# Kernel optimization log

Measured on AMD Instinct MI355X. Metric: run time of the kernel, lower is better.

Reference implementation:

```python
import jax, jax.numpy as jnp
import numpy as np

DIM = 1024
MLP_DIM = 4096
EPS = 1e-5


def layer_norm(x, gamma, beta):
    mean = jnp.mean(x, axis=-1, keepdims=True)
    var = jnp.mean(jnp.square(x - mean), axis=-1, keepdims=True)  # unbiased=False
    return gamma * (x - mean) / jnp.sqrt(var + EPS) + beta


def setup_inputs() -> dict:
    key = jax.random.key(0)
    ks = jax.random.split(key, 12)
    s = 0.02
    return {
        "x": jax.random.normal(ks[0], (4, 2048, DIM), dtype=jnp.float32),
        "gamma1": jnp.ones((DIM,), jnp.float32),
        "beta1": jnp.zeros((DIM,), jnp.float32),
        "gamma2": jnp.ones((DIM,), jnp.float32),
        "beta2": jnp.zeros((DIM,), jnp.float32),
        "Wq": jax.random.normal(ks[1], (DIM, DIM), jnp.float32) * s,
        "bq": jnp.zeros((DIM,), jnp.float32),
        "Wk": jax.random.normal(ks[2], (DIM, DIM), jnp.float32) * s,
        "bk": jnp.zeros((DIM,), jnp.float32),
        "Wv": jax.random.normal(ks[3], (DIM, DIM), jnp.float32) * s,
        "bv": jnp.zeros((DIM,), jnp.float32),
        "W1": jax.random.normal(ks[4], (DIM, MLP_DIM), jnp.float32) * s,
        "b1": jnp.zeros((MLP_DIM,), jnp.float32),
        "W2": jax.random.normal(ks[5], (MLP_DIM, DIM), jnp.float32) * s,
        "b2": jnp.zeros((DIM,), jnp.float32),
    }


def reference(x, gamma1, beta1, gamma2, beta2, Wq, bq, Wk, bk, Wv, bv, W1, b1, W2, b2):
    # Pre-LN attention sub-block (single-head manual attention over full dim)
    residual = x
    h = layer_norm(x, gamma1, beta1)
    q = h @ Wq + bq  # [B,S,D]
    k = h @ Wk + bk
    v = h @ Wv + bv
    scale = 1.0 / jnp.sqrt(jnp.asarray(q.shape[-1], q.dtype))
    scores = jnp.einsum("bsd,btd->bst", q, k) * scale  # [B,S,S]
    attn = jax.nn.softmax(scores, axis=-1)
    x = jnp.einsum("bst,btd->bsd", attn, v) + residual
    # Pre-LN MLP sub-block
    residual = x
    h = layer_norm(x, gamma2, beta2)
    h = jax.nn.gelu(h @ W1 + b1, approximate=False)  # torch F.gelu exact
    x = h @ W2 + b2 + residual
    return x
```

## Files before the change

### kernel.cpp

```cpp
#include <hip/hip_runtime.h>
#include <hip/hip_bf16.h>
#include <math.h>

typedef __bf16 bf16x8 __attribute__((ext_vector_type(8)));
typedef float  f32x4  __attribute__((ext_vector_type(4)));
typedef __hip_bfloat16 bf16;

#define DIM  1024
#define MLPD 4096
#define NB   4
#define SEQ  2048
#define ROWS (NB * SEQ)

__device__ __forceinline__ void gload_lds16(const void* g, void* l) {
  __builtin_amdgcn_global_load_lds(
      (__attribute__((address_space(1))) void*)(g),
      (__attribute__((address_space(3))) void*)(l), 16, 0, 0);
}

__device__ __forceinline__ void bar() {
  asm volatile("" ::: "memory");
  __builtin_amdgcn_s_barrier();
  asm volatile("" ::: "memory");
}

__device__ __forceinline__ void vm0() {
  asm volatile("s_waitcnt vmcnt(0)" ::: "memory");
}

__device__ __forceinline__ bf16 to_bf16(float v) { return __float2bfloat16(v); }
__device__ __forceinline__ bf16 to_bf16(bf16 v)  { return v; }

template <int EPI>
__global__ __launch_bounds__(256, 4) void gemm128(
    const bf16* __restrict__ A,  long aBatch, int lda,
    const bf16* __restrict__ Bt, long bBatch, int ldb,
    void* __restrict__ Cout,     long cBatch, int ldc,
    const float* __restrict__ bias,
    const float* __restrict__ resid, long rBatch, int ldr,
    int K, float scale)
{
  __shared__ char smem[2][16384];

  const int gx = gridDim.x, gy = gridDim.y;
  const int n = gx * gy * gridDim.z;
  const int f = blockIdx.x + gx * (blockIdx.y + gy * blockIdx.z);
  const int o = (f & 7) * (n >> 3) + (f >> 3);
  const int sx = gx >> 3;
  int st = o >> 6;
  const int w = o & 63;
  const int spz = sx * (gy >> 3);
  const int bz = st / spz; st -= bz * spz;
  const int sty = st / sx, stx = st - sty * sx;
  const int by = sty * 8 + (w >> 3), bx = stx * 8 + (w & 7);

  const long rowBase = (long)by * 128;
  const long colBase = (long)bx * 128;
  const long ldaB = (long)lda * 2, ldbB = (long)ldb * 2;
  const char* Ag = (const char*)(A + bz * aBatch + rowBase * lda);
  const char* Bg = (const char*)(Bt + bz * bBatch + colBase * ldb);

  const int tid  = threadIdx.x;
  const int lane = tid & 63;
  const int wave = tid >> 6;
  const int wm = wave >> 1, wn = wave & 1;
  const int fr = lane & 15, fq = lane >> 4;

  const int sslot = (fq ^ (fr & 3)) << 4;
  const int abase = ((wm * 64 + fr) << 6) + sslot;
  const int bbase = ((wn * 64 + fr) << 6) + sslot + 8192;

  const int c0   = wave * 2;
  const int swz  = ((lane & 3) ^ ((lane >> 2) & 3)) << 4;
  const int srow = lane >> 2;
  const char* aSrc0 = Ag + (long)(c0 * 16 + srow) * ldaB + swz;
  const char* aSrc1 = aSrc0 + 16 * ldaB;
  const char* bSrc0 = Bg + (long)(c0 * 16 + srow) * ldbB + swz;
  const char* bSrc1 = bSrc0 + 16 * ldbB;
  const int doff = c0 * 1024 + lane * 16;

  const int NT = K >> 5;
  f32x4 acc[4][4] = {};

#define STAGE(WB)                                                              \
  do {                                                                         \
    gload_lds16(aSrc0, &smem[WB][doff]);                                       \
    gload_lds16(aSrc1, &smem[WB][doff + 1024]);                                \
    gload_lds16(bSrc0, &smem[WB][8192 + doff]);                                \
    gload_lds16(bSrc1, &smem[WB][8192 + doff + 1024]);                         \
    aSrc0 += 64; aSrc1 += 64; bSrc0 += 64; bSrc1 += 64;                        \
  } while (0)

#define TILE(T, RB, WB)                                                        \
  do {                                                                         \
    if ((T) + 1 < NT) STAGE(WB);                                               \
    bf16x8 av[4], bv[4];                                                       \
    _Pragma("unroll") for (int m = 0; m < 4; ++m)                              \
      av[m] = *(const bf16x8*)(&smem[RB][0] + abase + m * 1024);               \
    _Pragma("unroll") for (int nn = 0; nn < 4; ++nn)                           \
      bv[nn] = *(const bf16x8*)(&smem[RB][0] + bbase + nn * 1024);             \
    __builtin_amdgcn_s_setprio(1);                                             \
    _Pragma("unroll") for (int m = 0; m < 4; ++m)                              \
      _Pragma("unroll") for (int nn = 0; nn < 4; ++nn)                         \
        acc[m][nn] = __builtin_amdgcn_mfma_f32_16x16x32_bf16(                  \
            av[m], bv[nn], acc[m][nn], 0, 0, 0);                               \
    __builtin_amdgcn_s_setprio(0);                                             \
    vm0(); bar();                                                              \
  } while (0)

  STAGE(0);
  vm0(); bar();

  for (int t = 0; t < NT; t += 2) {
    TILE(t, 0, 1);
    TILE(t + 1, 1, 0);
  }

#undef STAGE
#undef TILE

#pragma unroll
  for (int m = 0; m < 4; ++m) {
#pragma unroll
    for (int nn = 0; nn < 4; ++nn) {
      const long col = colBase + wn * 64 + nn * 16 + fr;
#pragma unroll
      for (int e = 0; e < 4; ++e) {
        const long r = rowBase + wm * 64 + m * 16 + fq * 4 + e;
        float v = acc[m][nn][e];
        if constexpr (EPI == 0) {
          v += bias[col];
          ((bf16*)Cout)[bz * cBatch + r * ldc + col] = __float2bfloat16(v);
        } else if constexpr (EPI == 1) {
          ((float*)Cout)[bz * cBatch + r * ldc + col] = v * scale;
        } else if constexpr (EPI == 2) {
          v += resid[bz * rBatch + r * ldr + col];
          ((float*)Cout)[bz * cBatch + r * ldc + col] = v;
        } else if constexpr (EPI == 3) {
          v += bias[col];
          const float gl = 0.5f * v * (1.0f + erff(v * 0.70710678118654752f));
          ((bf16*)Cout)[bz * cBatch + r * ldc + col] = __float2bfloat16(gl);
        } else {
          v += bias[col] + resid[r * (long)ldr + col];
          ((float*)Cout)[bz * cBatch + r * ldc + col] = v;
        }
      }
    }
  }
}

__global__ __launch_bounds__(256) void ln_kernel(
    const float* __restrict__ x, const float* __restrict__ gamma,
    const float* __restrict__ beta, bf16* __restrict__ out)
{
  const long row = blockIdx.x;
  const float4 v = ((const float4*)(x + row * DIM))[threadIdx.x];
  float s  = v.x + v.y + v.z + v.w;
  float ss = v.x * v.x + v.y * v.y + v.z * v.z + v.w * v.w;
  const int lane = threadIdx.x & 63, wave = threadIdx.x >> 6;
#pragma unroll
  for (int o = 32; o; o >>= 1) { s += __shfl_xor(s, o); ss += __shfl_xor(ss, o); }
  __shared__ float rs[4], rss[4];
  if (lane == 0) { rs[wave] = s; rss[wave] = ss; }
  __syncthreads();
  s  = rs[0] + rs[1] + rs[2] + rs[3];
  ss = rss[0] + rss[1] + rss[2] + rss[3];
  const float mean = s * (1.0f / DIM);
  const float var  = ss * (1.0f / DIM) - mean * mean;
  const float rstd = rsqrtf(var + 1e-5f);
  const float4 g = ((const float4*)gamma)[threadIdx.x];
  const float4 b = ((const float4*)beta)[threadIdx.x];
  union { bf16 h[4]; uint2 u; } pk;
  pk.h[0] = __float2bfloat16(g.x * (v.x - mean) * rstd + b.x);
  pk.h[1] = __float2bfloat16(g.y * (v.y - mean) * rstd + b.y);
  pk.h[2] = __float2bfloat16(g.z * (v.z - mean) * rstd + b.z);
  pk.h[3] = __float2bfloat16(g.w * (v.w - mean) * rstd + b.w);
  ((uint2*)(out + row * DIM))[threadIdx.x] = pk.u;
}

__global__ __launch_bounds__(256) void softmax_kernel(float* __restrict__ scores)
{
  const long row = blockIdx.x;
  float* rp = scores + row * (long)SEQ;
  const float4 v0 = ((const float4*)rp)[threadIdx.x * 2];
  const float4 v1 = ((const float4*)rp)[threadIdx.x * 2 + 1];
  float f[8] = {v0.x, v0.y, v0.z, v0.w, v1.x, v1.y, v1.z, v1.w};
  const int lane = threadIdx.x & 63, wave = threadIdx.x >> 6;
  float mx = f[0];
#pragma unroll
  for (int j = 1; j < 8; ++j) mx = fmaxf(mx, f[j]);
#pragma unroll
  for (int o = 32; o; o >>= 1) mx = fmaxf(mx, __shfl_xor(mx, o));
  __shared__ float rm[4], rsum[4];
  if (lane == 0) rm[wave] = mx;
  __syncthreads();
  mx = fmaxf(fmaxf(rm[0], rm[1]), fmaxf(rm[2], rm[3]));
  float sum = 0.0f;
#pragma unroll
  for (int j = 0; j < 8; ++j) { f[j] = expf(f[j] - mx); sum += f[j]; }
#pragma unroll
  for (int o = 32; o; o >>= 1) sum += __shfl_xor(sum, o);
  if (lane == 0) rsum[wave] = sum;
  __syncthreads();
  sum = rsum[0] + rsum[1] + rsum[2] + rsum[3];
  const float inv = 1.0f / sum;
  union { bf16 h[8]; uint4 u; } pk;
#pragma unroll
  for (int j = 0; j < 8; ++j) pk.h[j] = __float2bfloat16(f[j] * inv);
  bf16* prow = (bf16*)scores + row * (long)(2 * SEQ);
  ((uint4*)prow)[threadIdx.x] = pk.u;
}

template <typename TI>
__global__ __launch_bounds__(256) void transpose_bf16_kernel(
    const TI* __restrict__ in, bf16* __restrict__ out,
    int ldIn, int ldOut, long inBatch, long outBatch)
{
  __shared__ bf16 tile[32][33];
  const long zin  = (long)blockIdx.z * inBatch;
  const long zout = (long)blockIdx.z * outBatch;
  const int c0 = blockIdx.x * 32, r0 = blockIdx.y * 32;
  const int tx = threadIdx.x & 31, ty = threadIdx.x >> 5;
#pragma unroll
  for (int i = 0; i < 32; i += 8)
    tile[ty + i][tx] = to_bf16(in[zin + (long)(r0 + ty + i) * ldIn + c0 + tx]);
  __syncthreads();
#pragma unroll
  for (int i = 0; i < 32; i += 8)
    out[zout + (long)(c0 + ty + i) * ldOut + r0 + tx] = tile[tx][ty + i];
}

__global__ __launch_bounds__(256) void concat3_kernel(
    const float* __restrict__ a, const float* __restrict__ b,
    const float* __restrict__ c, float* __restrict__ o)
{
  const int i = blockIdx.x * 256 + threadIdx.x;
  if (i < DIM) { o[i] = a[i]; o[DIM + i] = b[i]; o[2 * DIM + i] = c[i]; }
}

extern "C" void kernel_launch(void* const* d_in, const int* in_sizes, int n_in,
                              void* d_out, int out_size, void* d_ws, size_t ws_size,
                              hipStream_t stream) {
  const float* x   = (const float*)d_in[0];
  const float* g1  = (const float*)d_in[1];
  const float* be1 = (const float*)d_in[2];
  const float* g2  = (const float*)d_in[3];
  const float* be2 = (const float*)d_in[4];
  const float* Wq  = (const float*)d_in[5];
  const float* bq  = (const float*)d_in[6];
  const float* Wk  = (const float*)d_in[7];
  const float* bk  = (const float*)d_in[8];
  const float* Wv  = (const float*)d_in[9];
  const float* bv  = (const float*)d_in[10];
  const float* W1  = (const float*)d_in[11];
  const float* b1  = (const float*)d_in[12];
  const float* W2  = (const float*)d_in[13];
  const float* b2  = (const float*)d_in[14];
  float* out = (float*)d_out;

  char* ws = (char*)d_ws;
  bf16* WqkvT = (bf16*)(ws + 0);
  bf16* W1T   = (bf16*)(ws + (6l << 20));
  bf16* W2T   = (bf16*)(ws + (14l << 20));
  float* bqkv = (float*)(ws + (22l << 20));
  bf16* h     = (bf16*)(ws + (23l << 20));
  bf16* qkv   = (bf16*)(ws + (39l << 20));
  bf16* vT    = (bf16*)(ws + (87l << 20));
  float* sc   = (float*)(ws + (103l << 20));
  bf16* P     = (bf16*)sc;
  bf16* g_act = (bf16*)sc;

  const dim3 blk(256);

  concat3_kernel<<<4, blk, 0, stream>>>(bq, bk, bv, bqkv);
  transpose_bf16_kernel<float><<<dim3(32, 32, 1), blk, 0, stream>>>(
      Wq, WqkvT, DIM, DIM, 0, 0);
  transpose_bf16_kernel<float><<<dim3(32, 32, 1), blk, 0, stream>>>(
      Wk, WqkvT + (long)DIM * DIM, DIM, DIM, 0, 0);
  transpose_bf16_kernel<float><<<dim3(32, 32, 1), blk, 0, stream>>>(
      Wv, WqkvT + 2l * DIM * DIM, DIM, DIM, 0, 0);
  transpose_bf16_kernel<float><<<dim3(128, 32, 1), blk, 0, stream>>>(
      W1, W1T, MLPD, DIM, 0, 0);
  transpose_bf16_kernel<float><<<dim3(32, 128, 1), blk, 0, stream>>>(
      W2, W2T, DIM, MLPD, 0, 0);

  ln_kernel<<<ROWS, blk, 0, stream>>>(x, g1, be1, h);

  gemm128<0><<<dim3(24, 64, 1), blk, 0, stream>>>(
      h, 0, DIM, WqkvT, 0, DIM, qkv, 0, 3 * DIM,
      bqkv, nullptr, 0, 0, DIM, 1.0f);

  transpose_bf16_kernel<bf16><<<dim3(32, 64, NB), blk, 0, stream>>>(
      qkv + 2 * DIM, vT, 3 * DIM, SEQ, (long)SEQ * 3 * DIM, (long)DIM * SEQ);

  gemm128<1><<<dim3(16, 16, NB), blk, 0, stream>>>(
      qkv, (long)SEQ * 3 * DIM, 3 * DIM, qkv + DIM, (long)SEQ * 3 * DIM, 3 * DIM,
      sc, (long)SEQ * SEQ, SEQ, nullptr, nullptr, 0, 0, DIM, 0.03125f);

  softmax_kernel<<<ROWS, blk, 0, stream>>>(sc);

  gemm128<2><<<dim3(8, 16, NB), blk, 0, stream>>>(
      P, (long)SEQ * 2 * SEQ, 2 * SEQ, vT, (long)DIM * SEQ, SEQ,
      out, (long)SEQ * DIM, DIM, nullptr, x, (long)SEQ * DIM, DIM, SEQ, 1.0f);

  ln_kernel<<<ROWS, blk, 0, stream>>>(out, g2, be2, h);

  gemm128<3><<<dim3(32, 64, 1), blk, 0, stream>>>(
      h, 0, DIM, W1T, 0, DIM, g_act, 0, MLPD, b1, nullptr, 0, 0, DIM, 1.0f);

  gemm128<4><<<dim3(8, 64, 1), blk, 0, stream>>>(
      g_act, 0, MLPD, W2T, 0, MLPD, out, 0, DIM, b2, out, 0, DIM, MLPD, 1.0f);
}
```

Measured before the change: 387.7 us.

## Triple-buffer GEMM LDS pipeline and store attention scores in bf16

```diff
diff --git a/kernel.cpp b/kernel.cpp
--- a/kernel.cpp
+++ b/kernel.cpp
@@ -24,15 +24,16 @@
   asm volatile("" ::: "memory");
 }
 
-__device__ __forceinline__ void vm0() {
-  asm volatile("s_waitcnt vmcnt(0)" ::: "memory");
+template <int N>
+__device__ __forceinline__ void vmw() {
+  asm volatile("s_waitcnt vmcnt(%0)" ::"n"(N) : "memory");
 }
 
 __device__ __forceinline__ bf16 to_bf16(float v) { return __float2bfloat16(v); }
 __device__ __forceinline__ bf16 to_bf16(bf16 v)  { return v; }
 
 template <int EPI>
-__global__ __launch_bounds__(256, 4) void gemm128(
+__global__ __launch_bounds__(256, 3) void gemm128(
     const bf16* __restrict__ A,  long aBatch, int lda,
     const bf16* __restrict__ Bt, long bBatch, int ldb,
     void* __restrict__ Cout,     long cBatch, int ldc,
@@ -40,7 +41,7 @@
     const float* __restrict__ resid, long rBatch, int ldr,
     int K, float scale)
 {
-  __shared__ char smem[2][16384];
+  __shared__ char smem[3][16384];
 
   const int gx = gridDim.x, gy = gridDim.y;
   const int n = gx * gy * gridDim.z;
@@ -66,58 +67,70 @@
   const int wm = wave >> 1, wn = wave & 1;
   const int fr = lane & 15, fq = lane >> 4;
 
-  const int sslot = (fq ^ (fr & 3)) << 4;
-  const int abase = ((wm * 64 + fr) << 6) + sslot;
-  const int bbase = ((wn * 64 + fr) << 6) + sslot + 8192;
-
-  const int c0   = wave * 2;
-  const int swz  = ((lane & 3) ^ ((lane >> 2) & 3)) << 4;
-  const int srow = lane >> 2;
-  const char* aSrc0 = Ag + (long)(c0 * 16 + srow) * ldaB + swz;
+  const int fh = fr >> 1;
+  const int sA = (((fr & 1) << 2) | fq) ^ fh;
+  const int laneRd = fh * 128 + sA * 16;
+  const int abase = wm * 4096 + laneRd;
+  const int bbase = 8192 + wn * 4096 + laneRd;
+
+  const int t0   = wave * 128 + lane;
+  const int r2   = t0 >> 3;
+  const int u0   = (t0 & 7) ^ (r2 & 7);
+  const int row0 = r2 * 2 + (u0 >> 2);
+  const int kc0  = u0 & 3;
+  const char* aSrc0 = Ag + (long)row0 * ldaB + kc0 * 16;
   const char* aSrc1 = aSrc0 + 16 * ldaB;
-  const char* bSrc0 = Bg + (long)(c0 * 16 + srow) * ldbB + swz;
+  const char* bSrc0 = Bg + (long)row0 * ldbB + kc0 * 16;
   const char* bSrc1 = bSrc0 + 16 * ldbB;
-  const int doff = c0 * 1024 + lane * 16;
+  const int doff = wave * 2048 + lane * 16;
 
   const int NT = K >> 5;
   f32x4 acc[4][4] = {};
 
 #define STAGE(WB)                                                              \
   do {                                                                         \
-    gload_lds16(aSrc0, &smem[WB][doff]);                                       \
-    gload_lds16(aSrc1, &smem[WB][doff + 1024]);                                \
-    gload_lds16(bSrc0, &smem[WB][8192 + doff]);                                \
-    gload_lds16(bSrc1, &smem[WB][8192 + doff + 1024]);                         \
+    char* _b = &smem[0][0] + (WB) * 16384;                                     \
+    gload_lds16(aSrc0, _b + doff);                                             \
+    gload_lds16(aSrc1, _b + doff + 1024);                                      \
+    gload_lds16(bSrc0, _b + 8192 + doff);                                      \
+    gload_lds16(bSrc1, _b + 8192 + doff + 1024);                               \
     aSrc0 += 64; aSrc1 += 64; bSrc0 += 64; bSrc1 += 64;                        \
   } while (0)
 
-#define TILE(T, RB, WB)                                                        \
+#define READMM(RB)                                                             \
   do {                                                                         \
-    if ((T) + 1 < NT) STAGE(WB);                                               \
+    const char* _r = &smem[0][0] + (RB) * 16384;                               \
     bf16x8 av[4], bv[4];                                                       \
     _Pragma("unroll") for (int m = 0; m < 4; ++m)                              \
-      av[m] = *(const bf16x8*)(&smem[RB][0] + abase + m * 1024);               \
+      av[m] = *(const bf16x8*)(_r + abase + m * 1024);                         \
     _Pragma("unroll") for (int nn = 0; nn < 4; ++nn)                           \
-      bv[nn] = *(const bf16x8*)(&smem[RB][0] + bbase + nn * 1024);             \
+      bv[nn] = *(const bf16x8*)(_r + bbase + nn * 1024);                       \
     __builtin_amdgcn_s_setprio(1);                                             \
     _Pragma("unroll") for (int m = 0; m < 4; ++m)                              \
       _Pragma("unroll") for (int nn = 0; nn < 4; ++nn)                         \
         acc[m][nn] = __builtin_amdgcn_mfma_f32_16x16x32_bf16(                  \
             av[m], bv[nn], acc[m][nn], 0, 0, 0);                               \
     __builtin_amdgcn_s_setprio(0);                                             \
-    vm0(); bar();                                                              \
   } while (0)
 
-  STAGE(0);
-  vm0(); bar();
-
-  for (int t = 0; t < NT; t += 2) {
-    TILE(t, 0, 1);
-    TILE(t + 1, 1, 0);
+  STAGE(0); STAGE(1);
+  vmw<4>(); bar();
+
+  int rb = 0, wb = 2;
+  for (int j = 0; j < NT - 2; ++j) {
+    STAGE(wb);
+    READMM(rb);
+    vmw<4>(); bar();
+    rb = (rb == 2) ? 0 : rb + 1;
+    wb = (wb == 2) ? 0 : wb + 1;
   }
+  READMM(rb);
+  vmw<0>(); bar();
+  rb = (rb == 2) ? 0 : rb + 1;
+  READMM(rb);
 
 #undef STAGE
-#undef TILE
+#undef READMM
 
 #pragma unroll
   for (int m = 0; m < 4; ++m) {
@@ -131,8 +144,6 @@
         if constexpr (EPI == 0) {
           v += bias[col];
           ((bf16*)Cout)[bz * cBatch + r * ldc + col] = __float2bfloat16(v);
-        } else if constexpr (EPI == 1) {
-          ((float*)Cout)[bz * cBatch + r * ldc + col] = v * scale;
         } else if constexpr (EPI == 2) {
           v += resid[bz * rBatch + r * ldr + col];
           ((float*)Cout)[bz * cBatch + r * ldc + col] = v;
@@ -140,9 +151,11 @@
           v += bias[col];
           const float gl = 0.5f * v * (1.0f + erff(v * 0.70710678118654752f));
           ((bf16*)Cout)[bz * cBatch + r * ldc + col] = __float2bfloat16(gl);
-        } else {
+        } else if constexpr (EPI == 4) {
           v += bias[col] + resid[r * (long)ldr + col];
           ((float*)Cout)[bz * cBatch + r * ldc + col] = v;
+        } else {
+          ((bf16*)Cout)[bz * cBatch + r * ldc + col] = __float2bfloat16(v * scale);
         }
       }
     }
@@ -178,13 +191,15 @@
   ((uint2*)(out + row * DIM))[threadIdx.x] = pk.u;
 }
 
-__global__ __launch_bounds__(256) void softmax_kernel(float* __restrict__ scores)
+__global__ __launch_bounds__(256) void softmax_kernel(bf16* __restrict__ scores)
 {
   const long row = blockIdx.x;
-  float* rp = scores + row * (long)SEQ;
-  const float4 v0 = ((const float4*)rp)[threadIdx.x * 2];
-  const float4 v1 = ((const float4*)rp)[threadIdx.x * 2 + 1];
-  float f[8] = {v0.x, v0.y, v0.z, v0.w, v1.x, v1.y, v1.z, v1.w};
+  bf16* rp = scores + row * (long)SEQ;
+  union { bf16 h[8]; uint4 u; } in;
+  in.u = ((const uint4*)rp)[threadIdx.x];
+  float f[8];
+#pragma unroll
+  for (int j = 0; j < 8; ++j) f[j] = __bfloat162float(in.h[j]);
   const int lane = threadIdx.x & 63, wave = threadIdx.x >> 6;
   float mx = f[0];
 #pragma unroll
@@ -207,8 +222,7 @@
   union { bf16 h[8]; uint4 u; } pk;
 #pragma unroll
   for (int j = 0; j < 8; ++j) pk.h[j] = __float2bfloat16(f[j] * inv);
-  bf16* prow = (bf16*)scores + row * (long)(2 * SEQ);
-  ((uint4*)prow)[threadIdx.x] = pk.u;
+  ((uint4*)rp)[threadIdx.x] = pk.u;
 }
 
 template <typename TI>
@@ -266,8 +280,7 @@
   bf16* h     = (bf16*)(ws + (23l << 20));
   bf16* qkv   = (bf16*)(ws + (39l << 20));
   bf16* vT    = (bf16*)(ws + (87l << 20));
-  float* sc   = (float*)(ws + (103l << 20));
-  bf16* P     = (bf16*)sc;
+  bf16* sc    = (bf16*)(ws + (103l << 20));
   bf16* g_act = (bf16*)sc;
 
   const dim3 blk(256);
@@ -293,14 +306,14 @@
   transpose_bf16_kernel<bf16><<<dim3(32, 64, NB), blk, 0, stream>>>(
       qkv + 2 * DIM, vT, 3 * DIM, SEQ, (long)SEQ * 3 * DIM, (long)DIM * SEQ);
 
-  gemm128<1><<<dim3(16, 16, NB), blk, 0, stream>>>(
+  gemm128<5><<<dim3(16, 16, NB), blk, 0, stream>>>(
       qkv, (long)SEQ * 3 * DIM, 3 * DIM, qkv + DIM, (long)SEQ * 3 * DIM, 3 * DIM,
       sc, (long)SEQ * SEQ, SEQ, nullptr, nullptr, 0, 0, DIM, 0.03125f);
 
   softmax_kernel<<<ROWS, blk, 0, stream>>>(sc);
 
   gemm128<2><<<dim3(8, 16, NB), blk, 0, stream>>>(
-      P, (long)SEQ * 2 * SEQ, 2 * SEQ, vT, (long)DIM * SEQ, SEQ,
+      sc, (long)SEQ * SEQ, SEQ, vT, (long)DIM * SEQ, SEQ,
       out, (long)SEQ * DIM, DIM, nullptr, x, (long)SEQ * DIM, DIM, SEQ, 1.0f);
 
   ln_kernel<<<ROWS, blk, 0, stream>>>(out, g2, be2, h);
```

Measured after the change: 392.3 us. About the same (+1.2%).
